# Performance work log

Measured on AMD Instinct MI355X. Metric: run time of the kernel, lower is better.

Reference implementation:

```python
import jax, jax.numpy as jnp
import numpy as np

N_NODES = 100000
N_EDGES = 1600000
IN_DIM = 128
HID_DIM = 128
N_MASK = 5000
N_CLASSES = 4


def gcn_layer(x, src, dst, edge_weight, W, b):
    """PyG GCNConv: x' = D^{-1/2} (A + I) D^{-1/2} (x W) + b, with edge weights."""
    n = x.shape[0]
    loop = jnp.arange(n, dtype=src.dtype)
    s = jnp.concatenate([src, loop])                      # [E+N]
    d = jnp.concatenate([dst, loop])                      # [E+N]
    w = jnp.concatenate([edge_weight, jnp.ones((n,), edge_weight.dtype)])
    deg = jax.ops.segment_sum(w, d, num_segments=n)       # weighted in-degree incl. self-loop
    dis = jnp.where(deg > 0, jax.lax.rsqrt(deg), 0.0)     # deg^{-1/2}, inf -> 0
    norm = dis[s] * w * dis[d]                            # [E+N]
    h = x @ W                                             # [N, H] small GEMM
    msg = h[s] * norm[:, None]                            # gather + scale  [E+N, H]
    out = jax.ops.segment_sum(msg, d, num_segments=n)     # scatter-add     [N, H]
    return out + b


def setup_inputs() -> dict:
    key = jax.random.key(0)
    ks = jax.random.split(key, 8)
    x = jax.random.normal(ks[0], (N_NODES, IN_DIM), dtype=jnp.float32)
    edge_weight = jax.random.uniform(ks[1], (N_EDGES,), dtype=jnp.float32)
    W1 = jax.random.normal(ks[2], (IN_DIM, HID_DIM), dtype=jnp.float32) * (1.0 / np.sqrt(IN_DIM))
    b1 = jnp.zeros((HID_DIM,), jnp.float32)
    W2 = jax.random.normal(ks[3], (HID_DIM, HID_DIM), dtype=jnp.float32) * (1.0 / np.sqrt(HID_DIM))
    b2 = jnp.zeros((HID_DIM,), jnp.float32)
    edge_index = jax.random.randint(ks[4], (2, N_EDGES), 0, N_NODES, dtype=jnp.int32)
    mask_idx = jax.random.randint(ks[5], (N_MASK,), 0, N_NODES, dtype=jnp.int32)
    y = jax.random.randint(ks[6], (N_NODES,), 0, N_CLASSES, dtype=jnp.int32)
    return {"x": x, "edge_weight": edge_weight, "W1": W1, "b1": b1,
            "W2": W2, "b2": b2, "edge_index": edge_index,
            "mask_idx": mask_idx, "y": y}


def reference(x, edge_weight, W1, b1, W2, b2, edge_index, mask_idx, y):
    src, dst = edge_index[0], edge_index[1]
    h = gcn_layer(x, src, dst, edge_weight, W1, b1)
    h = jax.nn.relu(h)
    # F.dropout(training=False) in eval mode is identity
    h = gcn_layer(h, src, dst, edge_weight, W2, b2)
    return h[mask_idx], y[mask_idx]
```

## Files before the change

kernel.cpp:

```cpp
#include <hip/hip_runtime.h>

constexpr int N = 100000;
constexpr int E = 1600000;
constexpr int D = 128;
constexpr int M = 5000;

constexpr int MF_BLKS = (N + 255) / 256;

constexpr int NBITS = 7;
constexpr int BUCKET = 1 << NBITS;
constexpr int NB  = (N + BUCKET - 1) / BUCKET;
constexpr int CAP = 3072;
constexpr int EBP = 8192;
constexpr int NPP = (E + EBP - 1) / EBP;
constexpr int PREP_BLKS = 32;
constexpr int MB_BLKS = (M + 255) / 256;

typedef __attribute__((ext_vector_type(8))) short bf16x8;
typedef __attribute__((ext_vector_type(4))) float f32x4;


__device__ __forceinline__ unsigned int pack_bf16x2(float a, float b) {
    unsigned int ua = __float_as_uint(a);
    unsigned int ub = __float_as_uint(b);
    ua = (ua + 0x7FFFu + ((ua >> 16) & 1u)) >> 16;
    ub = (ub + 0x7FFFu + ((ub >> 16) & 1u)) & 0xFFFF0000u;
    return ua | ub;
}
__device__ __forceinline__ unsigned short bf16_rne(float a) {
    unsigned int ua = __float_as_uint(a);
    return (unsigned short)((ua + 0x7FFFu + ((ua >> 16) & 1u)) >> 16);
}
__device__ __forceinline__ float bf16_lo(unsigned int u) { return __uint_as_float(u << 16); }
__device__ __forceinline__ float bf16_hi(unsigned int u) { return __uint_as_float(u & 0xFFFF0000u); }


__global__ __launch_bounds__(256) void k_misc0(const float* __restrict__ W1,
                                               unsigned int* __restrict__ Wt1,
                                               int* __restrict__ gCursor,
                                               const int* __restrict__ mask,
                                               unsigned int* __restrict__ maskbit,
                                               unsigned int* __restrict__ needed) {
    const int t = threadIdx.x;
    if (blockIdx.x < PREP_BLKS) {
        int idx = blockIdx.x * 256 + t;
        int n = idx >> 6, kk = idx & 63;
        float a = W1[(2 * kk) * D + n];
        float b = W1[(2 * kk + 1) * D + n];
        Wt1[idx] = pack_bf16x2(a, b);
    } else if (blockIdx.x == PREP_BLKS) {
#pragma unroll
        for (int g = 0; g < 4; ++g) {
            int pos = t * 4 + g;
            if (pos < NB) gCursor[pos] = pos * CAP;
        }
    } else {
        int i = (blockIdx.x - PREP_BLKS - 1) * 256 + t;
        if (i < M) {
            int n = mask[i];
            atomicOr(&maskbit[n >> 5], 1u << (n & 31));
            atomicOr(&needed[n >> 5], 1u << (n & 31));
        }
    }
}


__global__ __launch_bounds__(1024) void k_part(const int* __restrict__ src,
                                               const int* __restrict__ dst,
                                               const float* __restrict__ ew,
                                               int* __restrict__ gCursor,
                                               unsigned long long* __restrict__ tmp,
                                               const unsigned int* __restrict__ maskbit,
                                               unsigned int* __restrict__ needed) {
    __shared__ int cnt[NB];
    __shared__ int off[NB];
    __shared__ int rk[NB];
    const int t = threadIdx.x;
    for (int i = t; i < NB; i += 1024) { cnt[i] = 0; rk[i] = 0; }
    __syncthreads();

    const int eb = blockIdx.x * EBP;
    int d_[8], s_[8];
    float w_[8];
#pragma unroll
    for (int i = 0; i < 8; ++i) {
        int e = eb + t + i * 1024;
        if (e < E) {
            d_[i] = __builtin_nontemporal_load(dst + e);
            s_[i] = __builtin_nontemporal_load(src + e);
            w_[i] = __builtin_nontemporal_load(ew + e);
            atomicAdd(&cnt[d_[i] >> NBITS], 1);
        } else {
            d_[i] = -1;
        }
    }
    __syncthreads();

    for (int i = t; i < NB; i += 1024) {
        int c = cnt[i];
        if (c > 0) off[i] = atomicAdd(&gCursor[i], c);
    }
    __syncthreads();

#pragma unroll
    for (int i = 0; i < 8; ++i) {
        if (d_[i] >= 0) {
            int b = d_[i] >> NBITS;
            int r = atomicAdd(&rk[b], 1);
            int pos = off[b] + r;
            if (pos < (b + 1) * CAP) {
                unsigned long long rec =
                    ((unsigned long long)(unsigned int)__float_as_int(w_[i]) << 32) |
                    ((unsigned int)s_[i] << NBITS) | (unsigned int)(d_[i] & (BUCKET - 1));
                tmp[pos] = rec;
            }
            if ((maskbit[d_[i] >> 5] >> (d_[i] & 31)) & 1u)
                atomicOr(&needed[s_[i] >> 5], 1u << (s_[i] & 31));
        }
    }
}


union SMem {
    unsigned int Ws[128 * 68];
    float wsumL[BUCKET];
};


__device__ __forceinline__ void gemm_mfma_body(unsigned int* __restrict__ Ws,
                                               const float* __restrict__ Xin,
                                               const unsigned int* __restrict__ Wt,
                                               unsigned short* __restrict__ out, int blk) {
    const int t = threadIdx.x;
#pragma unroll
    for (int i = 0; i < 8; ++i) {
        int f4 = t + i * 256;
        int n = f4 >> 4;
        int k4 = f4 & 15;
        uint4 w = ((const uint4*)Wt)[f4];
        *(uint4*)(&Ws[n * 68 + k4 * 4]) = w;
    }
    __syncthreads();

    const int wv = t >> 6, lane = t & 63;
    const int q = lane >> 4, l15 = lane & 15;
    const int rowBase = blk * 256 + wv * 64;

    f32x4 acc[4][8] = {};
#pragma unroll
    for (int kc = 0; kc < 4; ++kc) {
        bf16x8 af[4];
#pragma unroll
        for (int rt = 0; rt < 4; ++rt) {
            int row = rowBase + rt * 16 + l15;
            if (row > N - 1) row = N - 1;
            union { uint4 u; bf16x8 v; } cv;
            const float* xr = Xin + (size_t)row * D + kc * 32 + q * 8;
            float4 x0 = *(const float4*)xr;
            float4 x1 = *(const float4*)(xr + 4);
            cv.u.x = pack_bf16x2(x0.x, x0.y);
            cv.u.y = pack_bf16x2(x0.z, x0.w);
            cv.u.z = pack_bf16x2(x1.x, x1.y);
            cv.u.w = pack_bf16x2(x1.z, x1.w);
            af[rt] = cv.v;
        }
#pragma unroll
        for (int ct = 0; ct < 8; ++ct) {
            union { uint4 u; bf16x8 v; } bv;
            bv.u = *(const uint4*)(&Ws[(ct * 16 + l15) * 68 + kc * 16 + q * 4]);
#pragma unroll
            for (int rt = 0; rt < 4; ++rt)
                acc[rt][ct] = __builtin_amdgcn_mfma_f32_16x16x32_bf16(af[rt], bv.v, acc[rt][ct], 0, 0, 0);
        }
    }

#pragma unroll
    for (int rt = 0; rt < 4; ++rt) {
#pragma unroll
        for (int ct = 0; ct < 8; ++ct) {
            int col = ct * 16 + l15;
#pragma unroll
            for (int r = 0; r < 4; ++r) {
                int row = rowBase + rt * 16 + q * 4 + r;
                if (row < N) out[(size_t)row * D + col] = bf16_rne(acc[rt][ct][r]);
            }
        }
    }
}


__global__ __launch_bounds__(256) void k_disA_g1(const unsigned long long* __restrict__ tmp,
                                                 const int* __restrict__ gCursor,
                                                 float* __restrict__ dis,
                                                 const float* __restrict__ x,
                                                 const unsigned int* __restrict__ Wt1,
                                                 unsigned short* __restrict__ A) {
    __shared__ SMem sm;
    const int t = threadIdx.x;
    if (blockIdx.x < NB) {
        const int bk = blockIdx.x;
        if (t < BUCKET) sm.wsumL[t] = 0.f;
        __syncthreads();
        const int segBeg = bk * CAP;
        int segLen = gCursor[bk] - segBeg;
        if (segLen > CAP) segLen = CAP;
        for (int e = t; e < segLen; e += 256) {
            unsigned long long rec = tmp[segBeg + e];
            atomicAdd(&sm.wsumL[(int)(rec & (BUCKET - 1))],
                      __uint_as_float((unsigned int)(rec >> 32)));
        }
        __syncthreads();
        if (t < BUCKET) {
            int node = bk * BUCKET + t;
            if (node < N) dis[node] = rsqrtf(1.0f + sm.wsumL[t]);
        }
    } else {
        gemm_mfma_body(sm.Ws, x, Wt1, A, blockIdx.x - NB);
    }
}


__global__ __launch_bounds__(512) void k_sort_agg(const unsigned long long* __restrict__ tmp,
                                                  const int* __restrict__ gCursor,
                                                  const float* __restrict__ dis,
                                                  const unsigned int* __restrict__ needed,
                                                  const unsigned int* __restrict__ maskbit,
                                                  const float* __restrict__ b,
                                                  const unsigned int* __restrict__ Hb,
                                                  int* __restrict__ rowStart,
                                                  int* __restrict__ rowLen,
                                                  int2* __restrict__ pairs,
                                                  unsigned int* __restrict__ outB) {
    __shared__ int2 lp[CAP];
    __shared__ int cnt[BUCKET];
    __shared__ int offL[BUCKET + 1];
    __shared__ int wl[BUCKET];
    __shared__ int waveS[2];
    __shared__ int nw, wcur;
    const int bk = blockIdx.x;
    const int t = threadIdx.x;
    const int segBeg = bk * CAP;
    int segLen = gCursor[bk] - segBeg;
    if (segLen > CAP) segLen = CAP;

    if (t == 0) { nw = 0; wcur = 0; offL[BUCKET] = segLen; }
    if (t < BUCKET) cnt[t] = 0;
    const uint4 mb4 = ((const uint4*)maskbit)[bk];
    __syncthreads();

    unsigned long long r_[6];
#pragma unroll
    for (int i = 0; i < 6; ++i) {
        int e = t + i * 512;
        if (e < segLen) {
            r_[i] = tmp[segBeg + e];
            atomicAdd(&cnt[(int)(r_[i] & (BUCKET - 1))], 1);
        }
    }
    __syncthreads();

    const int lane = t & 63;
    {
        const int wv2 = t >> 6;
        const int pv = (t < BUCKET) ? cnt[t] : 0;
        int v = pv;
        for (int o = 1; o < 64; o <<= 1) {
            int u = __shfl_up(v, o);
            if (lane >= o) v += u;
        }
        if (lane == 63 && wv2 < 2) waveS[wv2] = v;
        __syncthreads();
        if (t < BUCKET) {
            const int wb = (wv2 == 1) ? waveS[0] : 0;
            const int ex = wb + v - pv;
            offL[t] = ex;
            const int node = bk * BUCKET + t;
            if (node < N) {
                rowStart[node] = segBeg + ex;
                rowLen[node] = pv;
                if ((needed[node >> 5] >> (node & 31)) & 1u) {
                    int r = atomicAdd(&nw, 1);
                    wl[r] = t;
                }
            }
            cnt[t] = 0;
        }
    }
    __syncthreads();

#pragma unroll
    for (int i = 0; i < 6; ++i) {
        int e = t + i * 512;
        if (e < segLen) {
            unsigned long long rec = r_[i];
            int dl = (int)(rec & (BUCKET - 1));
            int s  = (int)((rec >> NBITS) & 0xFFFFF);
            float w = __uint_as_float((unsigned int)(rec >> 32));
            float v = w * dis[s];
            int r = atomicAdd(&cnt[dl], 1);
            int pos = offL[dl] + r;
            int2 pr = make_int2(s, __float_as_int(v));
            lp[pos] = pr;
            unsigned int mw = (dl < 32) ? mb4.x : (dl < 64) ? mb4.y : (dl < 96) ? mb4.z : mb4.w;
            if ((mw >> (dl & 31)) & 1u) pairs[segBeg + pos] = pr;
        }
    }
    __syncthreads();

    for (;;) {
        int idx;
        if (lane == 0) idx = atomicAdd(&wcur, 1);
        idx = __shfl(idx, 0);
        if (idx >= nw) break;
        const int nl = wl[idx];
        const int node = bk * BUCKET + nl;
        const int beg = offL[nl], end = offL[nl + 1];
        float ax = 0.f, ay = 0.f;
        int j = beg;
        for (; j + 7 < end; j += 8) {
            int2 p[8];
            unsigned int h[8];
#pragma unroll
            for (int i = 0; i < 8; ++i) p[i] = lp[j + i];
#pragma unroll
            for (int i = 0; i < 8; ++i) h[i] = Hb[(size_t)p[i].x * 64 + lane];
#pragma unroll
            for (int i = 0; i < 8; ++i) {
                float v = __int_as_float(p[i].y);
                ax += bf16_lo(h[i]) * v;
                ay += bf16_hi(h[i]) * v;
            }
        }
        for (; j < end; ++j) {
            int2 p0 = lp[j];
            unsigned int h0 = Hb[(size_t)p0.x * 64 + lane];
            float v0 = __int_as_float(p0.y);
            ax += bf16_lo(h0) * v0;
            ay += bf16_hi(h0) * v0;
        }
        float dd = dis[node];
        float sn = dd * dd;
        unsigned int hs = Hb[(size_t)node * 64 + lane];
        float2 bb = ((const float2*)b)[lane];
        float ox = fmaxf(ax * dd + bf16_lo(hs) * sn + bb.x, 0.f);
        float oy = fmaxf(ay * dd + bf16_hi(hs) * sn + bb.y, 0.f);
        __builtin_nontemporal_store(pack_bf16x2(ox, oy), outB + (size_t)node * 64 + lane);
    }
}


__global__ __launch_bounds__(256) void k_mask_out(const unsigned int* __restrict__ Hb,
                                                  const int2* __restrict__ pairs,
                                                  const int* __restrict__ rowStart,
                                                  const int* __restrict__ rowLen,
                                                  const float* __restrict__ dis,
                                                  const float* __restrict__ W2,
                                                  const float* __restrict__ b2,
                                                  const int* __restrict__ mask,
                                                  const int* __restrict__ y,
                                                  float* __restrict__ out) {
    __shared__ float w2s[64 * 132];
    __shared__ float rowL[4][128];
    const int t = threadIdx.x;
    const int wv = t >> 6, lane = t & 63;
    const int i = blockIdx.x * 4 + wv;
    const int node = mask[i];
    const int beg = rowStart[node], end = beg + rowLen[node];

    float ax = 0.f, ay = 0.f;
    int j = beg;
    for (; j + 7 < end; j += 8) {
        int2 p[8];
        unsigned int h[8];
#pragma unroll
        for (int ii = 0; ii < 8; ++ii) p[ii] = pairs[j + ii];
#pragma unroll
        for (int ii = 0; ii < 8; ++ii) h[ii] = Hb[(size_t)p[ii].x * 64 + lane];
#pragma unroll
        for (int ii = 0; ii < 8; ++ii) {
            float v = __int_as_float(p[ii].y);
            ax += bf16_lo(h[ii]) * v;
            ay += bf16_hi(h[ii]) * v;
        }
    }
    for (; j < end; ++j) {
        int2 p0 = pairs[j];
        unsigned int h0 = Hb[(size_t)p0.x * 64 + lane];
        float v0 = __int_as_float(p0.y);
        ax += bf16_lo(h0) * v0;
        ay += bf16_hi(h0) * v0;
    }
    {
        float dd = dis[node];
        float sn = dd * dd;
        unsigned int hs = Hb[(size_t)node * 64 + lane];
        rowL[wv][2 * lane]     = ax * dd + bf16_lo(hs) * sn;
        rowL[wv][2 * lane + 1] = ay * dd + bf16_hi(hs) * sn;
    }

    float2 bb = ((const float2*)b2)[lane];
    float acc0 = bb.x, acc1 = bb.y;
#pragma unroll
    for (int h0 = 0; h0 < 2; ++h0) {
        __syncthreads();
        for (int idx = t; idx < 2048; idx += 256) {
            float4 v = ((const float4*)W2)[h0 * 2048 + idx];
            int k = (idx * 4) >> 7, n = (idx * 4) & 127;
            *(float4*)(&w2s[k * 132 + n]) = v;
        }
        __syncthreads();
#pragma unroll 8
        for (int k = 0; k < 64; ++k) {
            float a = rowL[wv][h0 * 64 + k];
            float2 w = *(const float2*)(&w2s[k * 132 + 2 * lane]);
            acc0 += a * w.x;
            acc1 += a * w.y;
        }
    }
    ((float2*)(out + (size_t)i * D))[lane] = make_float2(acc0, acc1);
    if (lane == 0) out[(size_t)M * D + i] = (float)y[node];
}

extern "C" void kernel_launch(void* const* d_in, const int* in_sizes, int n_in,
                              void* d_out, int out_size, void* d_ws, size_t ws_size,
                              hipStream_t stream) {
    const float* x  = (const float*)d_in[0];
    const float* ew = (const float*)d_in[1];
    const float* W1 = (const float*)d_in[2];
    const float* b1 = (const float*)d_in[3];
    const float* W2 = (const float*)d_in[4];
    const float* b2 = (const float*)d_in[5];
    const int* eidx = (const int*)d_in[6];
    const int* mask = (const int*)d_in[7];
    const int* y    = (const int*)d_in[8];
    const int* src = eidx;
    const int* dst = eidx + E;

    char* ws = (char*)d_ws;
    float* dis      = (float*)(ws);
    int*   rowStart = (int*)(ws + (size_t)512 * 1024);
    int*   rowLen   = (int*)(ws + (size_t)1024 * 1024);
    unsigned int* maskbit = (unsigned int*)(ws + (size_t)1440 * 1024);
    unsigned int* needed  = (unsigned int*)(ws + (size_t)1456 * 1024);
    int*   gCursor  = (int*)(ws + (size_t)1472 * 1024);
    unsigned int* Wt1 = (unsigned int*)(ws + (size_t)1480 * 1024);
    int2*  pairs    = (int2*)(ws + (size_t)2 * 1024 * 1024);
    unsigned long long* tmp = (unsigned long long*)(ws + (size_t)22 * 1024 * 1024);
    unsigned short* A  = (unsigned short*)(ws + (size_t)42 * 1024 * 1024);
    unsigned short* B  = (unsigned short*)(ws + (size_t)68 * 1024 * 1024);

    (void)hipMemsetAsync(ws + (size_t)1440 * 1024, 0, (size_t)32 * 1024, stream);
    hipLaunchKernelGGL(k_misc0, dim3(PREP_BLKS + 1 + MB_BLKS), dim3(256), 0, stream,
                       W1, Wt1, gCursor, mask, maskbit, needed);

    hipLaunchKernelGGL(k_part, dim3(NPP), dim3(1024), 0, stream,
                       src, dst, ew, gCursor, tmp, maskbit, needed);

    hipLaunchKernelGGL(k_disA_g1, dim3(NB + MF_BLKS), dim3(256), 0, stream,
                       tmp, gCursor, dis, x, Wt1, A);

    hipLaunchKernelGGL(k_sort_agg, dim3(NB), dim3(512), 0, stream,
                       tmp, gCursor, dis, needed, maskbit, b1,
                       (const unsigned int*)A, rowStart, rowLen, pairs, (unsigned int*)B);

    hipLaunchKernelGGL(k_mask_out, dim3(M / 4), dim3(256), 0, stream,
                       (const unsigned int*)B, pairs, rowStart, rowLen, dis, W2, b2,
                       mask, y, (float*)d_out);
}
```

Measured before the change: 237.0 us.

## Fold prep kernel into partition launch and move needed-node scan later

Removes the separate prep kernel. Its W1 packing and mask-bit work now run as extra blocks of the partition kernel, and the bucket cursors become zero-based offsets cleared by the existing memset. The needed-source marking, which had to read the mask bitmap during partitioning, moves into a separate scan over dst/src inside the degree/GEMM kernel, where the bitmap is guaranteed complete. Edges per partition block are halved and GEMM blocks are scheduled first. The aim is one fewer launch and lighter partition blocks, at the cost of re-reading the edge arrays for the needed scan.

```diff
diff --git a/kernel.cpp b/kernel.cpp
--- a/kernel.cpp
+++ b/kernel.cpp
@@ -11,10 +11,11 @@
 constexpr int BUCKET = 1 << NBITS;
 constexpr int NB  = (N + BUCKET - 1) / BUCKET;
 constexpr int CAP = 3072;
-constexpr int EBP = 8192;
+constexpr int EBP = 4096;
 constexpr int NPP = (E + EBP - 1) / EBP;
-constexpr int PREP_BLKS = 32;
-constexpr int MB_BLKS = (M + 255) / 256;
+constexpr int PREP_BLKS = 8;
+constexpr int MB_BLKS = (M + 1023) / 1024;
+constexpr int SCAN_BLKS = (E + 4095) / 4096;
 
 typedef __attribute__((ext_vector_type(8))) short bf16x8;
 typedef __attribute__((ext_vector_type(4))) float f32x4;
@@ -35,55 +36,50 @@
 __device__ __forceinline__ float bf16_hi(unsigned int u) { return __uint_as_float(u & 0xFFFF0000u); }
 
 
-__global__ __launch_bounds__(256) void k_misc0(const float* __restrict__ W1,
-                                               unsigned int* __restrict__ Wt1,
-                                               int* __restrict__ gCursor,
-                                               const int* __restrict__ mask,
-                                               unsigned int* __restrict__ maskbit,
-                                               unsigned int* __restrict__ needed) {
-    const int t = threadIdx.x;
-    if (blockIdx.x < PREP_BLKS) {
-        int idx = blockIdx.x * 256 + t;
-        int n = idx >> 6, kk = idx & 63;
-        float a = W1[(2 * kk) * D + n];
-        float b = W1[(2 * kk + 1) * D + n];
-        Wt1[idx] = pack_bf16x2(a, b);
-    } else if (blockIdx.x == PREP_BLKS) {
-#pragma unroll
-        for (int g = 0; g < 4; ++g) {
-            int pos = t * 4 + g;
-            if (pos < NB) gCursor[pos] = pos * CAP;
-        }
-    } else {
-        int i = (blockIdx.x - PREP_BLKS - 1) * 256 + t;
-        if (i < M) {
-            int n = mask[i];
-            atomicOr(&maskbit[n >> 5], 1u << (n & 31));
-            atomicOr(&needed[n >> 5], 1u << (n & 31));
-        }
-    }
-}
-
-
 __global__ __launch_bounds__(1024) void k_part(const int* __restrict__ src,
                                                const int* __restrict__ dst,
                                                const float* __restrict__ ew,
                                                int* __restrict__ gCursor,
                                                unsigned long long* __restrict__ tmp,
-                                               const unsigned int* __restrict__ maskbit,
+                                               const float* __restrict__ W1,
+                                               unsigned int* __restrict__ Wt1,
+                                               const int* __restrict__ mask,
+                                               unsigned int* __restrict__ maskbit,
                                                unsigned int* __restrict__ needed) {
     __shared__ int cnt[NB];
     __shared__ int off[NB];
     __shared__ int rk[NB];
     const int t = threadIdx.x;
+
+    if (blockIdx.x >= NPP) {
+        const int bi = blockIdx.x - NPP;
+        if (bi < PREP_BLKS) {
+            int idx = bi * 1024 + t;
+            if (idx < 8192) {
+                int n = idx >> 6, kk = idx & 63;
+                float a = W1[(2 * kk) * D + n];
+                float b = W1[(2 * kk + 1) * D + n];
+                Wt1[idx] = pack_bf16x2(a, b);
+            }
+        } else {
+            int i = (bi - PREP_BLKS) * 1024 + t;
+            if (i < M) {
+                int n = mask[i];
+                atomicOr(&maskbit[n >> 5], 1u << (n & 31));
+                atomicOr(&needed[n >> 5], 1u << (n & 31));
+            }
+        }
+        return;
+    }
+
     for (int i = t; i < NB; i += 1024) { cnt[i] = 0; rk[i] = 0; }
     __syncthreads();
 
     const int eb = blockIdx.x * EBP;
-    int d_[8], s_[8];
-    float w_[8];
-#pragma unroll
-    for (int i = 0; i < 8; ++i) {
+    int d_[4], s_[4];
+    float w_[4];
+#pragma unroll
+    for (int i = 0; i < 4; ++i) {
         int e = eb + t + i * 1024;
         if (e < E) {
             d_[i] = __builtin_nontemporal_load(dst + e);
@@ -103,19 +99,17 @@
     __syncthreads();
 
 #pragma unroll
-    for (int i = 0; i < 8; ++i) {
+    for (int i = 0; i < 4; ++i) {
         if (d_[i] >= 0) {
             int b = d_[i] >> NBITS;
             int r = atomicAdd(&rk[b], 1);
-            int pos = off[b] + r;
-            if (pos < (b + 1) * CAP) {
+            int posr = off[b] + r;
+            if (posr < CAP) {
                 unsigned long long rec =
                     ((unsigned long long)(unsigned int)__float_as_int(w_[i]) << 32) |
                     ((unsigned int)s_[i] << NBITS) | (unsigned int)(d_[i] & (BUCKET - 1));
-                tmp[pos] = rec;
-            }
-            if ((maskbit[d_[i] >> 5] >> (d_[i] & 31)) & 1u)
-                atomicOr(&needed[s_[i] >> 5], 1u << (s_[i] & 31));
+                tmp[(size_t)b * CAP + posr] = rec;
+            }
         }
     }
 }
@@ -194,15 +188,21 @@
                                                  float* __restrict__ dis,
                                                  const float* __restrict__ x,
                                                  const unsigned int* __restrict__ Wt1,
-                                                 unsigned short* __restrict__ A) {
+                                                 unsigned short* __restrict__ A,
+                                                 const int* __restrict__ src,
+                                                 const int* __restrict__ dst,
+                                                 const unsigned int* __restrict__ maskbit,
+                                                 unsigned int* __restrict__ needed) {
     __shared__ SMem sm;
     const int t = threadIdx.x;
-    if (blockIdx.x < NB) {
-        const int bk = blockIdx.x;
+    if (blockIdx.x < MF_BLKS) {
+        gemm_mfma_body(sm.Ws, x, Wt1, A, blockIdx.x);
+    } else if (blockIdx.x < MF_BLKS + NB) {
+        const int bk = blockIdx.x - MF_BLKS;
         if (t < BUCKET) sm.wsumL[t] = 0.f;
         __syncthreads();
-        const int segBeg = bk * CAP;
-        int segLen = gCursor[bk] - segBeg;
+        const size_t segBeg = (size_t)bk * CAP;
+        int segLen = gCursor[bk];
         if (segLen > CAP) segLen = CAP;
         for (int e = t; e < segLen; e += 256) {
             unsigned long long rec = tmp[segBeg + e];
@@ -215,7 +215,18 @@
             if (node < N) dis[node] = rsqrtf(1.0f + sm.wsumL[t]);
         }
     } else {
-        gemm_mfma_body(sm.Ws, x, Wt1, A, blockIdx.x - NB);
+        const int base = (blockIdx.x - MF_BLKS - NB) * 4096;
+#pragma unroll
+        for (int i = 0; i < 16; ++i) {
+            int e = base + t + i * 256;
+            if (e < E) {
+                int d = __builtin_nontemporal_load(dst + e);
+                if ((maskbit[d >> 5] >> (d & 31)) & 1u) {
+                    int s = src[e];
+                    atomicOr(&needed[s >> 5], 1u << (s & 31));
+                }
+            }
+        }
     }
 }
 
@@ -239,8 +250,8 @@
     __shared__ int nw, wcur;
     const int bk = blockIdx.x;
     const int t = threadIdx.x;
-    const int segBeg = bk * CAP;
-    int segLen = gCursor[bk] - segBeg;
+    const size_t segBeg = (size_t)bk * CAP;
+    int segLen = gCursor[bk];
     if (segLen > CAP) segLen = CAP;
 
     if (t == 0) { nw = 0; wcur = 0; offL[BUCKET] = segLen; }
@@ -276,7 +287,7 @@
             offL[t] = ex;
             const int node = bk * BUCKET + t;
             if (node < N) {
-                rowStart[node] = segBeg + ex;
+                rowStart[node] = (int)segBeg + ex;
                 rowLen[node] = pv;
                 if ((needed[node >> 5] >> (node & 31)) & 1u) {
                     int r = atomicAdd(&nw, 1);
@@ -449,15 +460,13 @@
     unsigned short* A  = (unsigned short*)(ws + (size_t)42 * 1024 * 1024);
     unsigned short* B  = (unsigned short*)(ws + (size_t)68 * 1024 * 1024);
 
-    (void)hipMemsetAsync(ws + (size_t)1440 * 1024, 0, (size_t)32 * 1024, stream);
-    hipLaunchKernelGGL(k_misc0, dim3(PREP_BLKS + 1 + MB_BLKS), dim3(256), 0, stream,
-                       W1, Wt1, gCursor, mask, maskbit, needed);
-
-    hipLaunchKernelGGL(k_part, dim3(NPP), dim3(1024), 0, stream,
-                       src, dst, ew, gCursor, tmp, maskbit, needed);
-
-    hipLaunchKernelGGL(k_disA_g1, dim3(NB + MF_BLKS), dim3(256), 0, stream,
-                       tmp, gCursor, dis, x, Wt1, A);
+    (void)hipMemsetAsync(ws + (size_t)1440 * 1024, 0, (size_t)36 * 1024, stream);
+
+    hipLaunchKernelGGL(k_part, dim3(NPP + PREP_BLKS + MB_BLKS), dim3(1024), 0, stream,
+                       src, dst, ew, gCursor, tmp, W1, Wt1, mask, maskbit, needed);
+
+    hipLaunchKernelGGL(k_disA_g1, dim3(MF_BLKS + NB + SCAN_BLKS), dim3(256), 0, stream,
+                       tmp, gCursor, dis, x, Wt1, A, src, dst, maskbit, needed);
 
     hipLaunchKernelGGL(k_sort_agg, dim3(NB), dim3(512), 0, stream,
                        tmp, gCursor, dis, needed, maskbit, b1,
```

After: 256.3 us. 8.1% more time.
